# Performance work log

Hardware: AMD Instinct MI355X
Metric: run time of the kernel (lower is better)

## Reference

```python
import jax, jax.numpy as jnp
import numpy as np

DIM = 512
HEADS = 8
HD = DIM // HEADS

def _rotate_half(t):
    t1, t2 = jnp.split(t, 2, axis=-1)
    return jnp.concatenate((-t2, t1), axis=-1)

def _layernorm(x, g, b, eps=1e-5):
    mu = jnp.mean(x, axis=-1, keepdims=True)
    var = jnp.var(x, axis=-1, keepdims=True)
    return (x - mu) * jax.lax.rsqrt(var + eps) * g + b

def setup_inputs() -> dict:
    key = jax.random.key(0)
    ks = jax.random.split(key, 12)
    B, S = 4, 2048
    x = jax.random.normal(ks[0], (B, S, DIM), dtype=jnp.float32)
    rope_cos = jax.random.uniform(ks[1], (1, S, 1, HD), dtype=jnp.float32)
    rope_sin = jax.random.uniform(ks[2], (1, S, 1, HD), dtype=jnp.float32)
    sd = 1.0 / np.sqrt(DIM)
    params = {
        'norm1_g': jnp.ones((DIM,), jnp.float32),
        'norm1_b': jnp.zeros((DIM,), jnp.float32),
        'norm2_g': jnp.ones((DIM,), jnp.float32),
        'norm2_b': jnp.zeros((DIM,), jnp.float32),
        'w_qkv': jax.random.uniform(ks[3], (DIM, 3 * DIM), jnp.float32, -sd, sd),
        'b_qkv': jax.random.uniform(ks[4], (3 * DIM,), jnp.float32, -sd, sd),
        'w_proj': jax.random.uniform(ks[5], (DIM, DIM), jnp.float32, -sd, sd),
        'b_proj': jax.random.uniform(ks[6], (DIM,), jnp.float32, -sd, sd),
        'w_fc1': jax.random.uniform(ks[7], (DIM, 4 * DIM), jnp.float32, -sd, sd),
        'b_fc1': jax.random.uniform(ks[8], (4 * DIM,), jnp.float32, -sd, sd),
        'w_fc2': jax.random.uniform(ks[9], (4 * DIM, DIM), jnp.float32, -1.0 / np.sqrt(4 * DIM), 1.0 / np.sqrt(4 * DIM)),
        'b_fc2': jax.random.uniform(ks[10], (DIM,), jnp.float32, -1.0 / np.sqrt(4 * DIM), 1.0 / np.sqrt(4 * DIM)),
    }
    return {'x': x, 'rope_cos': rope_cos, 'rope_sin': rope_sin, **params}

def reference(x, rope_cos, rope_sin, norm1_g, norm1_b, norm2_g, norm2_b,
              w_qkv, b_qkv, w_proj, b_proj, w_fc1, b_fc1, w_fc2, b_fc2):
    B, S, D = x.shape
    scale = 1.0 / np.sqrt(HD)
    shortcut = x
    h = _layernorm(x, norm1_g, norm1_b)
    qkv = (h @ w_qkv + b_qkv).reshape(B, S, 3, HEADS, HD)
    q, k, v = qkv[:, :, 0], qkv[:, :, 1], qkv[:, :, 2]  # [B,S,H,hd]
    q = q * rope_cos + _rotate_half(q) * rope_sin
    k = k * rope_cos + _rotate_half(k) * rope_sin
    # attention over heads: scores [B,H,S,S]
    attn = jnp.einsum('bqhd,bkhd->bhqk', q, k) * scale
    attn = jax.nn.softmax(attn, axis=-1)
    o = jnp.einsum('bhqk,bkhd->bqhd', attn, v).reshape(B, S, D)
    o = o @ w_proj + b_proj
    x = shortcut + o  # dropout is identity in eval
    h2 = _layernorm(x, norm2_g, norm2_b)
    mlp = jax.nn.gelu(h2 @ w_fc1 + b_fc1, approximate=False) @ w_fc2 + b_fc2
    return x + mlp
```

## Files before the change

kernel.cpp:

```cpp
#include <hip/hip_runtime.h>
#include <cstdint>
#include <cstddef>

typedef unsigned short u16;
typedef unsigned int   u32;
typedef __bf16 bf16x8 __attribute__((ext_vector_type(8)));
typedef float  f32x4  __attribute__((ext_vector_type(4)));

#define BS   8192
#define DIMM 512
#define NH   8
#define HD   64
#define SEQ  2048
#define DFF  2048
#define NQKV 1536

#define GLD16(g, l) __builtin_amdgcn_global_load_lds( \
    (__attribute__((address_space(1))) const void*)(g), \
    (__attribute__((address_space(3))) void*)(l), 16, 0, 0)

__device__ __forceinline__ float b2f(u16 s) {
  u32 u = ((u32)s) << 16;
  float f; __builtin_memcpy(&f, &u, 4); return f;
}
__device__ __forceinline__ u16 f2b(float f) {
  u32 u; __builtin_memcpy(&u, &f, 4);
  u += 0x7fffu + ((u >> 16) & 1u);
  return (u16)(u >> 16);
}
__device__ __forceinline__ u16 f2b_rtz(float f) {
  u32 u; __builtin_memcpy(&u, &f, 4);
  return (u16)(u >> 16);
}

#define SZ_QKV (DIMM * NQKV)
#define SZ_PRJ (DIMM * DIMM)
#define SZ_F1  (DIMM * DFF)
#define SZ_F2  (DFF * DIMM)
__global__ __launch_bounds__(256) void transpose_all_k(
    const float* __restrict__ w_qkv, const float* __restrict__ w_prj,
    const float* __restrict__ w_f1,  const float* __restrict__ w_f2,
    u16* __restrict__ o_qkv, u16* __restrict__ o_prj,
    u16* __restrict__ o_f1,  u16* __restrict__ o_f2) {
  int idx = blockIdx.x * 256 + threadIdx.x;
  const float* W; u16* O; int Kd, Nd, off;
  if (idx < SZ_QKV)                         { W = w_qkv; O = o_qkv; Kd = DIMM; Nd = NQKV; off = idx; }
  else if (idx < SZ_QKV + SZ_PRJ)           { W = w_prj; O = o_prj; Kd = DIMM; Nd = DIMM; off = idx - SZ_QKV; }
  else if (idx < SZ_QKV + SZ_PRJ + SZ_F1)   { W = w_f1;  O = o_f1;  Kd = DIMM; Nd = DFF;  off = idx - SZ_QKV - SZ_PRJ; }
  else                                      { W = w_f2;  O = o_f2;  Kd = DFF;  Nd = DIMM; off = idx - SZ_QKV - SZ_PRJ - SZ_F1; }
  int n = off / Kd, k = off - n * Kd;
  O[off] = f2b(W[(size_t)k * Nd + n]);
}

__global__ __launch_bounds__(256) void ln_f32b_k(const float* __restrict__ X,
    const float* __restrict__ G, const float* __restrict__ Bb, u16* __restrict__ out) {
  int w = threadIdx.x >> 6, lane = threadIdx.x & 63;
  size_t row = (size_t)blockIdx.x * 4 + w;
  const float* xr = X + row * DIMM;
  float v[8];
  *(float4*)&v[0] = *(const float4*)(xr + lane * 8);
  *(float4*)&v[4] = *(const float4*)(xr + lane * 8 + 4);
  float s = 0.f, s2 = 0.f;
#pragma unroll
  for (int j = 0; j < 8; j++) { s += v[j]; s2 += v[j] * v[j]; }
#pragma unroll
  for (int m = 1; m < 64; m <<= 1) { s += __shfl_xor(s, m); s2 += __shfl_xor(s2, m); }
  float mu = s * (1.f / DIMM);
  float rsd = rsqrtf(s2 * (1.f / DIMM) - mu * mu + 1e-5f);
  float g[8], bb[8];
  *(float4*)&g[0]  = *(const float4*)(G + lane * 8);
  *(float4*)&g[4]  = *(const float4*)(G + lane * 8 + 4);
  *(float4*)&bb[0] = *(const float4*)(Bb + lane * 8);
  *(float4*)&bb[4] = *(const float4*)(Bb + lane * 8 + 4);
  uint4 ov; u16* os = (u16*)&ov;
#pragma unroll
  for (int j = 0; j < 8; j++) os[j] = f2b((v[j] - mu) * rsd * g[j] + bb[j]);
  *(uint4*)(out + row * DIMM + lane * 8) = ov;
}

template <int EPI, int TM>
__global__ __launch_bounds__(256) void gemm_bt(const u16* __restrict__ A,
    const u16* __restrict__ BT, const float* __restrict__ bias,
    void* __restrict__ Cout, const float* __restrict__ resid, int N, int Kd) {
  __shared__ u16 a_s[TM * 32];
  __shared__ u16 b_s[128 * 32];
  int t = threadIdx.x, lane = t & 63, w = t >> 6;
  int l15 = lane & 15, quad = lane >> 4;
  int gx = gridDim.x;
  int lid = blockIdx.x + gx * blockIdx.y;
  int per = (gx * gridDim.y) >> 3;
  int nid = (lid & 7) * per + (lid >> 3);
  int bx = nid % gx, by = nid / gx;
  int m0 = by * TM, n0 = bx * 128;
  constexpr int MT = TM / 32;
  int wm = (w >> 1) * (TM / 2), wn = (w & 1) * 64;
  f32x4 z4 = {0.f, 0.f, 0.f, 0.f};
  f32x4 acc[MT][4];
#pragma unroll
  for (int i = 0; i < MT; i++)
#pragma unroll
    for (int j = 0; j < 4; j++) acc[i][j] = z4;

  for (int k0 = 0; k0 < Kd; k0 += 32) {
    __syncthreads();
#pragma unroll
    for (int i = 0; i < TM / 64; i++) {
      int c = t + i * 256;
      int row = c >> 2, ch = c & 3;
      GLD16(A + (size_t)(m0 + row) * Kd + k0 + ch * 8, &a_s[c * 8]);
    }
#pragma unroll
    for (int i = 0; i < 2; i++) {
      int c = t + i * 256;
      int row = c >> 2, ch = c & 3;
      GLD16(BT + (size_t)(n0 + row) * Kd + k0 + ch * 8, &b_s[c * 8]);
    }
    __syncthreads();
    bf16x8 af[MT], bfm[4];
#pragma unroll
    for (int mt = 0; mt < MT; mt++) af[mt] = *(const bf16x8*)&a_s[(wm + mt * 16 + l15) * 32 + quad * 8];
#pragma unroll
    for (int nt = 0; nt < 4; nt++) bfm[nt] = *(const bf16x8*)&b_s[(wn + nt * 16 + l15) * 32 + quad * 8];
#pragma unroll
    for (int mt = 0; mt < MT; mt++)
#pragma unroll
      for (int nt = 0; nt < 4; nt++)
        acc[mt][nt] = __builtin_amdgcn_mfma_f32_16x16x32_bf16(af[mt], bfm[nt], acc[mt][nt], 0, 0, 0);
  }

#pragma unroll
  for (int nt = 0; nt < 4; nt++) {
    int col = n0 + wn + nt * 16 + l15;
    float bv = bias[col];
#pragma unroll
    for (int mt = 0; mt < MT; mt++) {
#pragma unroll
      for (int r = 0; r < 4; r++) {
        int rw = m0 + wm + mt * 16 + quad * 4 + r;
        float v = acc[mt][nt][r] + bv;
        size_t off = (size_t)rw * N + col;
        if (EPI == 0) {
          ((float*)Cout)[off] = v;
        } else if (EPI == 1) {
          ((float*)Cout)[off] = v + resid[off];
        } else if (EPI == 2) {
          ((u16*)Cout)[off] = f2b(0.5f * v * (1.f + erff(v * 0.70710678118654752f)));
        } else {
          ((u16*)Cout)[off] = f2b(v);
        }
      }
    }
  }
}

#define QSCALE 0.18033688f
__global__ __launch_bounds__(256) void rope_k(const u16* __restrict__ qkv,
    const float* __restrict__ C, const float* __restrict__ Sn,
    u16* __restrict__ Qo, u16* __restrict__ Ko, u16* __restrict__ Vo) {
  int idx = blockIdx.x * 256 + threadIdx.x;
  int row = idx / 192;
  int cn = idx - row * 192;
  int n0 = cn * 8;
  int comp = n0 >> 9;
  int hh = (n0 >> 6) & 7;
  int d0 = n0 & 63;
  int b = row >> 11, s = row & 2047;
  const u16* src = qkv + (size_t)row * NQKV;
  uint4 val = *(const uint4*)(src + n0);
  u16* vs = (u16*)&val;
  size_t oo = ((size_t)((b << 3) + hh) * SEQ + s) * HD + d0;
  if (comp == 2) { *(uint4*)(Vo + oo) = val; return; }
  uint4 pv = *(const uint4*)(src + (n0 ^ 32));
  u16* ps = (u16*)&pv;
  float cv[8], sv[8];
  *(float4*)&cv[0] = *(const float4*)(C + s * HD + d0);
  *(float4*)&cv[4] = *(const float4*)(C + s * HD + d0 + 4);
  *(float4*)&sv[0] = *(const float4*)(Sn + s * HD + d0);
  *(float4*)&sv[4] = *(const float4*)(Sn + s * HD + d0 + 4);
  float sgn = (d0 & 32) ? 1.f : -1.f;
  float sc = (comp == 0) ? QSCALE : 1.f;
  uint4 ov; u16* os = (u16*)&ov;
#pragma unroll
  for (int j = 0; j < 8; j++)
    os[j] = f2b(sc * (b2f(vs[j]) * cv[j] + sgn * b2f(ps[j]) * sv[j]));
  *(uint4*)((comp == 0 ? Qo : Ko) + oo) = ov;
}

__global__ __launch_bounds__(256) void attn_flash_k(const u16* __restrict__ Qg,
    const u16* __restrict__ Kg, const u16* __restrict__ Vg, u16* __restrict__ Og) {
  __shared__ u16 q_s[128 * 72];
  __shared__ u16 k_s[64 * 72];
  __shared__ u16 vt_s[64 * 72];
  int t = threadIdx.x, lane = t & 63, w = t >> 6;
  int l15 = lane & 15, quad = lane >> 4;
  int lid = blockIdx.x;
  int nid = (lid & 7) * 64 + (lid >> 3);
  int bh = nid >> 4;
  int qt0 = (nid & 15) * 128;
  int b = bh >> 3, h = bh & 7;
  const u16* Qp = Qg + (size_t)bh * SEQ * HD;
  const u16* Kp = Kg + (size_t)bh * SEQ * HD;
  const u16* Vp = Vg + (size_t)bh * SEQ * HD;
  int row0 = t >> 3, ch = t & 7;
  int row1 = row0 + 32;
  int r8a = row0 >> 3, r0a = row0 & 7;
  int r8b = row1 >> 3, r0b = row1 & 7;

#pragma unroll
  for (int i = 0; i < 4; i++) {
    int c = t + i * 256, qr = c >> 3, qc = c & 7;
    *(uint4*)&q_s[qr * 72 + qc * 8] = *(const uint4*)(Qp + (size_t)(qt0 + qr) * HD + qc * 8);
  }
  uint4 kr0 = *(const uint4*)(Kp + (size_t)row0 * HD + ch * 8);
  uint4 kr1 = *(const uint4*)(Kp + (size_t)row1 * HD + ch * 8);
  uint4 vr0 = *(const uint4*)(Vp + (size_t)row0 * HD + ch * 8);
  uint4 vr1 = *(const uint4*)(Vp + (size_t)row1 * HD + ch * 8);
  __syncthreads();
  bf16x8 qa[2][2];
#pragma unroll
  for (int rs = 0; rs < 2; rs++) {
    qa[rs][0] = *(const bf16x8*)&q_s[(rs * 64 + w * 16 + l15) * 72 + quad * 8];
    qa[rs][1] = *(const bf16x8*)&q_s[(rs * 64 + w * 16 + l15) * 72 + 32 + quad * 8];
  }
  u16* p_s = q_s;
  f32x4 z4 = {0.f, 0.f, 0.f, 0.f};
  f32x4 of[2][4];
#pragma unroll
  for (int rs = 0; rs < 2; rs++)
#pragma unroll
    for (int n = 0; n < 4; n++) of[rs][n] = z4;
  float lrun[2][4] = {};

  for (int kt = 0; kt < SEQ; kt += 64) {
    __syncthreads();
    *(uint4*)&k_s[row0 * 72 + ch * 8] = kr0;
    *(uint4*)&k_s[row1 * 72 + ch * 8] = kr1;
    {
      u16* v0 = (u16*)&vr0; u16* v1 = (u16*)&vr1;
#pragma unroll
      for (int j = 0; j < 8; j++) {
        int d = ch * 8 + j;
        vt_s[d * 72 + ((r8a ^ ch) << 3) + r0a] = v0[j];
        vt_s[d * 72 + ((r8b ^ ch) << 3) + r0b] = v1[j];
      }
    }
    __syncthreads();
    if (kt + 64 < SEQ) {
      kr0 = *(const uint4*)(Kp + (size_t)(kt + 64 + row0) * HD + ch * 8);
      kr1 = *(const uint4*)(Kp + (size_t)(kt + 64 + row1) * HD + ch * 8);
      vr0 = *(const uint4*)(Vp + (size_t)(kt + 64 + row0) * HD + ch * 8);
      vr1 = *(const uint4*)(Vp + (size_t)(kt + 64 + row1) * HD + ch * 8);
    }
    f32x4 sf[2][4];
#pragma unroll
    for (int rs = 0; rs < 2; rs++)
#pragma unroll
      for (int n = 0; n < 4; n++) sf[rs][n] = z4;
#pragma unroll
    for (int kk = 0; kk < 2; kk++)
#pragma unroll
      for (int n = 0; n < 4; n++) {
        bf16x8 kb = *(const bf16x8*)&k_s[(n * 16 + l15) * 72 + kk * 32 + quad * 8];
        sf[0][n] = __builtin_amdgcn_mfma_f32_16x16x32_bf16(qa[0][kk], kb, sf[0][n], 0, 0, 0);
        sf[1][n] = __builtin_amdgcn_mfma_f32_16x16x32_bf16(qa[1][kk], kb, sf[1][n], 0, 0, 0);
      }
#pragma unroll
    for (int rs = 0; rs < 2; rs++)
#pragma unroll
      for (int r = 0; r < 4; r++) {
        int prow = (rs * 64 + w * 16 + quad * 4 + r) * 72;
#pragma unroll
        for (int n = 0; n < 4; n++) {
          float pp = exp2f(sf[rs][n][r]);
          lrun[rs][r] += pp;
          p_s[prow + n * 16 + l15] = f2b_rtz(pp);
        }
      }
#pragma unroll
    for (int kk = 0; kk < 2; kk++) {
      bf16x8 pa0 = *(const bf16x8*)&p_s[(w * 16 + l15) * 72 + kk * 32 + quad * 8];
      bf16x8 pa1 = *(const bf16x8*)&p_s[(64 + w * 16 + l15) * 72 + kk * 32 + quad * 8];
#pragma unroll
      for (int n = 0; n < 4; n++) {
        bf16x8 vb = *(const bf16x8*)&vt_s[(n * 16 + l15) * 72 +
                     (((kk * 4 + quad) ^ (2 * n + (l15 >> 3))) << 3)];
        of[0][n] = __builtin_amdgcn_mfma_f32_16x16x32_bf16(pa0, vb, of[0][n], 0, 0, 0);
        of[1][n] = __builtin_amdgcn_mfma_f32_16x16x32_bf16(pa1, vb, of[1][n], 0, 0, 0);
      }
    }
  }
#pragma unroll
  for (int rs = 0; rs < 2; rs++)
#pragma unroll
    for (int r = 0; r < 4; r++) {
      float l = lrun[rs][r];
#pragma unroll
      for (int m = 1; m < 16; m <<= 1) l += __shfl_xor(l, m);
      float inv = 1.f / l;
      size_t orow = (size_t)(b * SEQ + qt0 + rs * 64 + w * 16 + quad * 4 + r);
#pragma unroll
      for (int n = 0; n < 4; n++)
        Og[orow * DIMM + h * HD + n * 16 + l15] = f2b(of[rs][n][r] * inv);
    }
}

extern "C" void kernel_launch(void* const* d_in, const int* in_sizes, int n_in,
                              void* d_out, int out_size, void* d_ws, size_t ws_size,
                              hipStream_t stream) {
  const float* x    = (const float*)d_in[0];
  const float* rc   = (const float*)d_in[1];
  const float* rsn  = (const float*)d_in[2];
  const float* n1g  = (const float*)d_in[3];
  const float* n1b  = (const float*)d_in[4];
  const float* n2g  = (const float*)d_in[5];
  const float* n2b  = (const float*)d_in[6];
  const float* wqkv = (const float*)d_in[7];
  const float* bqkv = (const float*)d_in[8];
  const float* wprj = (const float*)d_in[9];
  const float* bprj = (const float*)d_in[10];
  const float* wf1  = (const float*)d_in[11];
  const float* bf1  = (const float*)d_in[12];
  const float* wf2  = (const float*)d_in[13];
  const float* bf2  = (const float*)d_in[14];

  char* p = (char*)d_ws;
  u16*   wqkvT = (u16*)p;
  u16*   wprjT = (u16*)(p + (2u  << 20));
  u16*   wf1T  = (u16*)(p + (3u  << 20));
  u16*   wf2T  = (u16*)(p + (5u  << 20));
  u16*   h1    = (u16*)(p + (8u  << 20));
  u16*   qkvb  = (u16*)(p + (16u << 20));
  u16*   Qb    = (u16*)(p + (64u << 20));
  u16*   Kb    = (u16*)(p + (72u << 20));
  u16*   Vb    = (u16*)(p + (80u << 20));
  float* x2    = (float*)(p + (88u << 20));
  u16*   ob    = h1;
  u16*   h2    = h1;
  u16*   mid   = qkvb;

  transpose_all_k<<<dim3((SZ_QKV + SZ_PRJ + SZ_F1 + SZ_F2) / 256), 256, 0, stream>>>(
      wqkv, wprj, wf1, wf2, wqkvT, wprjT, wf1T, wf2T);

  ln_f32b_k<<<dim3(BS / 4), 256, 0, stream>>>(x, n1g, n1b, h1);

  gemm_bt<3, 128><<<dim3(NQKV / 128, BS / 128), 256, 0, stream>>>(h1, wqkvT, bqkv, qkvb, nullptr, NQKV, DIMM);

  rope_k<<<dim3(BS * NQKV / 8 / 256), 256, 0, stream>>>(qkvb, rc, rsn, Qb, Kb, Vb);

  attn_flash_k<<<dim3(32 * (SEQ / 128)), 256, 0, stream>>>(Qb, Kb, Vb, ob);

  gemm_bt<1, 64><<<dim3(DIMM / 128, BS / 64), 256, 0, stream>>>(ob, wprjT, bprj, x2, x, DIMM, DIMM);

  ln_f32b_k<<<dim3(BS / 4), 256, 0, stream>>>(x2, n2g, n2b, h2);

  gemm_bt<2, 128><<<dim3(DFF / 128, BS / 128), 256, 0, stream>>>(h2, wf1T, bf1, mid, nullptr, DFF, DIMM);

  gemm_bt<1, 64><<<dim3(DIMM / 128, BS / 64), 256, 0, stream>>>(mid, wf2T, bf2, (float*)d_out, x2, DIMM, DFF);
}
```

Before: 317.0 us.

## Split attention key range in two with separate combine kernel

Each query tile's key sequence is split into two halves processed by separate blocks, doubling the attention grid to improve CU occupancy. Unnormalized fp32 partial outputs and row sums are written to workspace, and a new combine kernel sums them, normalizes, and writes bf16. This relies on the softmax having no running max, so partials add directly. It adds extra fp32 traffic and a kernel launch.

Measured after the change: 324.5 us. 1.02x slower.

```diff
diff --git a/kernel.cpp b/kernel.cpp
--- a/kernel.cpp
+++ b/kernel.cpp
@@ -6,6 +6,7 @@
 typedef unsigned int   u32;
 typedef __bf16 bf16x8 __attribute__((ext_vector_type(8)));
 typedef float  f32x4  __attribute__((ext_vector_type(4)));
+typedef u16    u16x4  __attribute__((ext_vector_type(4)));
 
 #define BS   8192
 #define DIMM 512
@@ -187,17 +188,21 @@
 }
 
 __global__ __launch_bounds__(256) void attn_flash_k(const u16* __restrict__ Qg,
-    const u16* __restrict__ Kg, const u16* __restrict__ Vg, u16* __restrict__ Og) {
+    const u16* __restrict__ Kg, const u16* __restrict__ Vg,
+    float* __restrict__ Op, float* __restrict__ Lp) {
   __shared__ u16 q_s[128 * 72];
   __shared__ u16 k_s[64 * 72];
   __shared__ u16 vt_s[64 * 72];
   int t = threadIdx.x, lane = t & 63, w = t >> 6;
   int l15 = lane & 15, quad = lane >> 4;
   int lid = blockIdx.x;
-  int nid = (lid & 7) * 64 + (lid >> 3);
-  int bh = nid >> 4;
-  int qt0 = (nid & 15) * 128;
+  int nid = (lid & 7) * 128 + (lid >> 3);
+  int split = nid & 1;
+  int rest = nid >> 1;
+  int bh = rest >> 4;
+  int qt0 = (rest & 15) * 128;
   int b = bh >> 3, h = bh & 7;
+  int kbase = split * (SEQ / 2);
   const u16* Qp = Qg + (size_t)bh * SEQ * HD;
   const u16* Kp = Kg + (size_t)bh * SEQ * HD;
   const u16* Vp = Vg + (size_t)bh * SEQ * HD;
@@ -211,10 +216,10 @@
     int c = t + i * 256, qr = c >> 3, qc = c & 7;
     *(uint4*)&q_s[qr * 72 + qc * 8] = *(const uint4*)(Qp + (size_t)(qt0 + qr) * HD + qc * 8);
   }
-  uint4 kr0 = *(const uint4*)(Kp + (size_t)row0 * HD + ch * 8);
-  uint4 kr1 = *(const uint4*)(Kp + (size_t)row1 * HD + ch * 8);
-  uint4 vr0 = *(const uint4*)(Vp + (size_t)row0 * HD + ch * 8);
-  uint4 vr1 = *(const uint4*)(Vp + (size_t)row1 * HD + ch * 8);
+  uint4 kr0 = *(const uint4*)(Kp + (size_t)(kbase + row0) * HD + ch * 8);
+  uint4 kr1 = *(const uint4*)(Kp + (size_t)(kbase + row1) * HD + ch * 8);
+  uint4 vr0 = *(const uint4*)(Vp + (size_t)(kbase + row0) * HD + ch * 8);
+  uint4 vr1 = *(const uint4*)(Vp + (size_t)(kbase + row1) * HD + ch * 8);
   __syncthreads();
   bf16x8 qa[2][2];
 #pragma unroll
@@ -231,7 +236,7 @@
     for (int n = 0; n < 4; n++) of[rs][n] = z4;
   float lrun[2][4] = {};
 
-  for (int kt = 0; kt < SEQ; kt += 64) {
+  for (int kt = kbase; kt < kbase + SEQ / 2; kt += 64) {
     __syncthreads();
     *(uint4*)&k_s[row0 * 72 + ch * 8] = kr0;
     *(uint4*)&k_s[row1 * 72 + ch * 8] = kr1;
@@ -245,7 +250,7 @@
       }
     }
     __syncthreads();
-    if (kt + 64 < SEQ) {
+    if (kt + 64 < kbase + SEQ / 2) {
       kr0 = *(const uint4*)(Kp + (size_t)(kt + 64 + row0) * HD + ch * 8);
       kr1 = *(const uint4*)(Kp + (size_t)(kt + 64 + row1) * HD + ch * 8);
       vr0 = *(const uint4*)(Vp + (size_t)(kt + 64 + row0) * HD + ch * 8);
@@ -289,19 +294,39 @@
       }
     }
   }
+  float* Ob = Op + (size_t)split * BS * DIMM;
+  float* Lb = Lp + (size_t)split * (BS * NH / 8);
 #pragma unroll
   for (int rs = 0; rs < 2; rs++)
 #pragma unroll
     for (int r = 0; r < 4; r++) {
+      int qrow = qt0 + rs * 64 + w * 16 + quad * 4 + r;
       float l = lrun[rs][r];
 #pragma unroll
       for (int m = 1; m < 16; m <<= 1) l += __shfl_xor(l, m);
-      float inv = 1.f / l;
-      size_t orow = (size_t)(b * SEQ + qt0 + rs * 64 + w * 16 + quad * 4 + r);
+      if (l15 == 0) Lb[(size_t)bh * SEQ + qrow] = l;
+      size_t orow = (size_t)(b * SEQ + qrow);
 #pragma unroll
       for (int n = 0; n < 4; n++)
-        Og[orow * DIMM + h * HD + n * 16 + l15] = f2b(of[rs][n][r] * inv);
-    }
+        Ob[orow * DIMM + h * HD + n * 16 + l15] = of[rs][n][r];
+    }
+}
+
+__global__ __launch_bounds__(256) void combine_k(const float* __restrict__ Op,
+    const float* __restrict__ Lp, u16* __restrict__ ob) {
+  int idx = (blockIdx.x * 256 + threadIdx.x) * 4;
+  int row = idx >> 9, col = idx & 511;
+  int b = row >> 11, q = row & 2047, h = col >> 6;
+  size_t li = (size_t)(b * NH + h) * SEQ + q;
+  float inv = 1.f / (Lp[li] + Lp[(size_t)BS * NH / 8 * 1 + li]);
+  float4 o1 = *(const float4*)(Op + (size_t)idx);
+  float4 o2 = *(const float4*)(Op + (size_t)BS * DIMM + idx);
+  u16x4 ov;
+  ov[0] = f2b((o1.x + o2.x) * inv);
+  ov[1] = f2b((o1.y + o2.y) * inv);
+  ov[2] = f2b((o1.z + o2.z) * inv);
+  ov[3] = f2b((o1.w + o2.w) * inv);
+  *(u16x4*)(ob + idx) = ov;
 }
 
 extern "C" void kernel_launch(void* const* d_in, const int* in_sizes, int n_in,
@@ -330,6 +355,8 @@
   u16*   wf2T  = (u16*)(p + (5u  << 20));
   u16*   h1    = (u16*)(p + (8u  << 20));
   u16*   qkvb  = (u16*)(p + (16u << 20));
+  float* Opart = (float*)(p + (16u << 20));
+  float* Lpart = (float*)(p + (48u << 20));
   u16*   Qb    = (u16*)(p + (64u << 20));
   u16*   Kb    = (u16*)(p + (72u << 20));
   u16*   Vb    = (u16*)(p + (80u << 20));
@@ -347,7 +374,9 @@
 
   rope_k<<<dim3(BS * NQKV / 8 / 256), 256, 0, stream>>>(qkvb, rc, rsn, Qb, Kb, Vb);
 
-  attn_flash_k<<<dim3(32 * (SEQ / 128)), 256, 0, stream>>>(Qb, Kb, Vb, ob);
+  attn_flash_k<<<dim3(2 * 32 * (SEQ / 128)), 256, 0, stream>>>(Qb, Kb, Vb, Opart, Lpart);
+
+  combine_k<<<dim3(BS * DIMM / 4 / 256), 256, 0, stream>>>(Opart, Lpart, ob);
 
   gemm_bt<1, 64><<<dim3(DIMM / 128, BS / 64), 256, 0, stream>>>(ob, wprjT, bprj, x2, x, DIMM, DIMM);
 
```
